# Performance work log

Measured on AMD Instinct MI355X. Metric: run time of the kernel, lower is better.

Reference implementation:

```python
import jax, jax.numpy as jnp
import numpy as np

FEATURE_DIM = 6272
UNITS = 32
B, L = 8, 256

def setup_inputs() -> dict:
    key = jax.random.key(0)
    k1, k2, k3, k4, k5 = jax.random.split(key, 5)
    return {
        "inputs": jax.random.normal(k1, (B, L, FEATURE_DIM), dtype=jnp.float32),
        "Wt": jax.random.normal(k2, (FEATURE_DIM, UNITS), dtype=jnp.float32) * 0.02,
        "bh": jax.random.normal(k3, (UNITS,), dtype=jnp.float32),
        "Wa": jax.random.normal(k4, (UNITS, 1), dtype=jnp.float32) * 0.02,
        "ba": jax.random.normal(k5, (1,), dtype=jnp.float32),
    }

def reference(inputs, Wt, bh, Wa, ba):
    # q == k: both projected through Wt (original code reuses Wt for both)
    p = jnp.einsum('blf,fu->blu', inputs, Wt)            # [B, L, U]
    # additive (Bahdanau-style) pairwise combine: [B, L, L, U]
    beta = jnp.tanh(p[:, :, None, :] + p[:, None, :, :] + bh)
    alpha = jnp.einsum('bqku,uo->bqk', beta, Wa) + ba[0]  # [B, L, L]
    alpha = jax.nn.sigmoid(alpha)
    a = jax.nn.softmax(alpha, axis=-1)                    # softmax over keys
    c_r = jnp.einsum('bqk,bkf->bqf', a, inputs)           # [B, L, F]
    return c_r
```

## Files before the change

kernel.cpp:

```cpp
#include <hip/hip_runtime.h>
#include <hip/hip_bf16.h>
#include <math.h>

#define FDIM 6272
#define LQ   256
#define BN   8
#define UDIM 32
#define BL   (BN*LQ)

typedef short  short8 __attribute__((ext_vector_type(8)));
typedef float  f32x4  __attribute__((ext_vector_type(4)));

static __device__ __forceinline__ ushort f2bf(float f) {
    __hip_bfloat16 h = __float2bfloat16(f);
    return *(ushort*)&h;
}
static __device__ __forceinline__ float fexp2(float x) {
    float r;
    asm volatile("v_exp_f32 %0, %1 \n s_nop 1" : "=v"(r) : "v"(x));
    return r;
}
static __device__ __forceinline__ float frcp(float x) {
    float r;
    asm volatile("v_rcp_f32 %0, %1 \n s_nop 1" : "=v"(r) : "v"(x));
    return r;
}
static __device__ __forceinline__ float tanh_fast(float v) {
    return 1.f - 2.f * frcp(1.f + fexp2(v * 2.88539008177793f));
}

__global__ __launch_bounds__(256)
void k_wtt(const float* __restrict__ Wt, ushort* __restrict__ wtt,
           float* __restrict__ pb) {
    const int gid = blockIdx.x * 256 + threadIdx.x;
    const int u = gid / 784, fg = gid % 784;
    ushort v[8];
    #pragma unroll
    for (int j = 0; j < 8; ++j)
        v[j] = f2bf(Wt[(size_t)(8 * fg + j) * UDIM + u]);
    *(uint4*)(wtt + (size_t)u * FDIM + 8 * fg) = *(uint4*)v;

    if (gid < BL * UDIM / 4)
        ((float4*)pb)[gid] = make_float4(0.f, 0.f, 0.f, 0.f);
}

__global__ __launch_bounds__(256)
void k1_mfma(const float* __restrict__ x, const ushort* __restrict__ wtt,
             float* __restrict__ pb, ushort* __restrict__ xb16) {
    const int t    = threadIdx.x;
    const int wv   = t >> 6, lane = t & 63;
    const int n16  = lane & 15, quad = lane >> 4;
    const int row0 = blockIdx.x * 32 + 16 * (wv & 1);
    const int u0   = 16 * (wv >> 1);
    const int f0   = blockIdx.y * 896;

    const float*  xr = x    + (size_t)(row0 + n16) * FDIM + f0 + quad * 8;
    const ushort* wr = wtt  + (size_t)(u0   + n16) * FDIM + f0 + quad * 8;
    ushort*       xw = xb16 + (size_t)(row0 + n16) * FDIM + f0 + quad * 8;

    f32x4 acc = (f32x4){0.f, 0.f, 0.f, 0.f};

    #pragma unroll 4
    for (int c = 0; c < 28; ++c) {
        const float4 a0 = *(const float4*)(xr + c * 32);
        const float4 a1 = *(const float4*)(xr + c * 32 + 4);
        short8 af;
        af[0] = (short)f2bf(a0.x); af[1] = (short)f2bf(a0.y);
        af[2] = (short)f2bf(a0.z); af[3] = (short)f2bf(a0.w);
        af[4] = (short)f2bf(a1.x); af[5] = (short)f2bf(a1.y);
        af[6] = (short)f2bf(a1.z); af[7] = (short)f2bf(a1.w);
        if (wv < 2)
            *(short8*)(xw + c * 32) = af;
        const short8 bf = *(const short8*)(wr + c * 32);
        acc = __builtin_amdgcn_mfma_f32_16x16x32_bf16(af, bf, acc, 0, 0, 0);
    }

    #pragma unroll
    for (int r = 0; r < 4; ++r)
        atomicAdd(&pb[(size_t)(row0 + quad * 4 + r) * UDIM + u0 + n16], acc[r]);
}

__global__ __launch_bounds__(256)
void k2_attn(const float* __restrict__ pb, const float* __restrict__ bh,
             const float* __restrict__ Wa, const float* __restrict__ ba,
             ushort* __restrict__ ab) {
    const int bq = blockIdx.x;
    const int b  = bq >> 8, q = bq & 255;
    const int k  = threadIdx.x;

    __shared__ float pk_s[LQ * 33];
    __shared__ float pq_s[UDIM];
    __shared__ float wa_s[UDIM];
    __shared__ float red[4];

    if (k < UDIM) wa_s[k] = Wa[k];
    const float* pbb = pb + (size_t)b * LQ * UDIM;
    #pragma unroll
    for (int i = 0; i < 32; ++i) {
        int idx = k + i * 256;
        pk_s[(idx >> 5) * 33 + (idx & 31)] = pbb[idx];
    }
    __syncthreads();
    if (k < UDIM) pq_s[k] = pk_s[q * 33 + k] + bh[k];
    __syncthreads();

    const float* pk = &pk_s[k * 33];
    float s = 0.f;
    #pragma unroll
    for (int u = 0; u < UDIM; ++u)
        s = fmaf(tanh_fast(pq_s[u] + pk[u]), wa_s[u], s);

    const float alpha = frcp(1.f + fexp2(-(s + ba[0]) * 1.44269504088896f));
    const float e = fexp2(alpha * 1.44269504088896f);

    float v = e;
    #pragma unroll
    for (int m = 1; m < 64; m <<= 1) v += __shfl_xor(v, m, 64);
    if ((k & 63) == 0) red[k >> 6] = v;
    __syncthreads();
    const float tot = red[0] + red[1] + red[2] + red[3];

    ab[(size_t)bq * LQ + k] = f2bf(e * frcp(tot));
}

__global__ __launch_bounds__(256)
void k3_fused(const ushort* __restrict__ xb16, const ushort* __restrict__ ab,
              float* __restrict__ out) {
    __shared__ ushort Bs[2][64 * 72];

    const int t    = threadIdx.x;
    const int f0   = blockIdx.x * 64;
    const int b    = blockIdx.y;
    const int wv   = t >> 6;
    const int lane = t & 63;
    const int n16  = lane & 15;
    const int quad = lane >> 4;
    const int g    = t >> 4;
    const int kp   = t & 15;

    const ushort* xb  = xb16 + (size_t)b * LQ * FDIM + f0 + 4 * g;
    const ushort* abb = ab   + (size_t)b * LQ * LQ;

    f32x4 acc[4][4];
    #pragma unroll
    for (int mf = 0; mf < 4; ++mf)
        #pragma unroll
        for (int nf = 0; nf < 4; ++nf)
            acc[mf][nf] = (f32x4){0.f, 0.f, 0.f, 0.f};

    uint2 r0, r1, r2, r3;
#define LDX(kc) do {                                                      \
        r0 = *(const uint2*)(xb + (size_t)((kc) + 2 * kp     ) * FDIM);   \
        r1 = *(const uint2*)(xb + (size_t)((kc) + 2 * kp +  1) * FDIM);   \
        r2 = *(const uint2*)(xb + (size_t)((kc) + 2 * kp + 32) * FDIM);   \
        r3 = *(const uint2*)(xb + (size_t)((kc) + 2 * kp + 33) * FDIM);   \
    } while (0)
#define STX(bufi) do {                                                    \
        unsigned* bw = (unsigned*)(Bs[bufi]);                             \
        bw[(4 * g + 0) * 36 + kp]      = (r0.x & 0xffffu) | (r1.x << 16); \
        bw[(4 * g + 1) * 36 + kp]      = (r0.x >> 16) | (r1.x & 0xffff0000u); \
        bw[(4 * g + 2) * 36 + kp]      = (r0.y & 0xffffu) | (r1.y << 16); \
        bw[(4 * g + 3) * 36 + kp]      = (r0.y >> 16) | (r1.y & 0xffff0000u); \
        bw[(4 * g + 0) * 36 + kp + 16] = (r2.x & 0xffffu) | (r3.x << 16); \
        bw[(4 * g + 1) * 36 + kp + 16] = (r2.x >> 16) | (r3.x & 0xffff0000u); \
        bw[(4 * g + 2) * 36 + kp + 16] = (r2.y & 0xffffu) | (r3.y << 16); \
        bw[(4 * g + 3) * 36 + kp + 16] = (r2.y >> 16) | (r3.y & 0xffff0000u); \
    } while (0)

    LDX(0);
    STX(0);

    for (int c = 0; c < 4; ++c) {
        if (c < 3) LDX((c + 1) * 64);
        short8 af[4][2];
        #pragma unroll
        for (int mf = 0; mf < 4; ++mf)
            #pragma unroll
            for (int h = 0; h < 2; ++h)
                af[mf][h] = *(const short8*)(abb
                    + (size_t)(64 * wv + 16 * mf + n16) * LQ
                    + c * 64 + h * 32 + quad * 8);
        __syncthreads();
        const ushort* bsc = Bs[c & 1];
        #pragma unroll
        for (int h = 0; h < 2; ++h)
            #pragma unroll
            for (int nf = 0; nf < 4; ++nf) {
                const short8 bf = *(const short8*)(bsc + (16 * nf + n16) * 72
                                                   + h * 32 + quad * 8);
                #pragma unroll
                for (int mf = 0; mf < 4; ++mf)
                    acc[mf][nf] = __builtin_amdgcn_mfma_f32_16x16x32_bf16(
                        af[mf][h], bf, acc[mf][nf], 0, 0, 0);
            }
        if (c < 3) STX((c + 1) & 1);
    }
#undef LDX
#undef STX

    float* ob = out + ((size_t)b * LQ + 64 * wv + quad * 4) * FDIM + f0 + n16;
    #pragma unroll
    for (int mf = 0; mf < 4; ++mf)
        #pragma unroll
        for (int nf = 0; nf < 4; ++nf)
            #pragma unroll
            for (int r = 0; r < 4; ++r)
                ob[(size_t)(16 * mf + r) * FDIM + 16 * nf] = acc[mf][nf][r];
}

extern "C" void kernel_launch(void* const* d_in, const int* in_sizes, int n_in,
                              void* d_out, int out_size, void* d_ws, size_t ws_size,
                              hipStream_t stream) {
    const float* x  = (const float*)d_in[0];
    const float* Wt = (const float*)d_in[1];
    const float* bh = (const float*)d_in[2];
    const float* Wa = (const float*)d_in[3];
    const float* ba = (const float*)d_in[4];
    float* out = (float*)d_out;

    float*  pb   = (float*)d_ws;
    ushort* ab   = (ushort*)((char*)d_ws + 262144);
    ushort* wtt  = (ushort*)((char*)d_ws + 262144 + 1048576);
    ushort* xb16 = (ushort*)((char*)d_ws + 262144 + 1048576 + 524288);

    k_wtt<<<98, 256, 0, stream>>>(Wt, wtt, pb);
    k1_mfma<<<dim3(64, 7), 256, 0, stream>>>(x, wtt, pb, xb16);
    k2_attn<<<BL, 256, 0, stream>>>(pb, bh, Wa, ba, ab);
    k3_fused<<<dim3(98, 8), 256, 0, stream>>>(xb16, ab, out);
}
```

Before: 163.1 us.

## Factor tanh via exp products and batch queries per block in attention kernel

The attention-score kernel rewrites tanh(pq+pk+bh) using precomputed exponentials: exp(2pk) is computed once per key and exp(2bh) once per unit, so each pair costs one FMA and one reciprocal instead of an exp plus a reciprocal. Each block now handles four queries per batch, so the key projection staging and exponentials are reused across queries. The projection kernel also splits the feature dimension into twice as many chunks for more parallelism, at the cost of more atomics. The exp-product form can overflow for large projections, which risks inf/NaN handling differences.

```diff
diff --git a/kernel.cpp b/kernel.cpp
--- a/kernel.cpp
+++ b/kernel.cpp
@@ -7,6 +7,7 @@
 #define BN   8
 #define UDIM 32
 #define BL   (BN*LQ)
+#define QG   4
 
 typedef short  short8 __attribute__((ext_vector_type(8)));
 typedef float  f32x4  __attribute__((ext_vector_type(4)));
@@ -24,9 +25,6 @@
     float r;
     asm volatile("v_rcp_f32 %0, %1 \n s_nop 1" : "=v"(r) : "v"(x));
     return r;
-}
-static __device__ __forceinline__ float tanh_fast(float v) {
-    return 1.f - 2.f * frcp(1.f + fexp2(v * 2.88539008177793f));
 }
 
 __global__ __launch_bounds__(256)
@@ -52,7 +50,7 @@
     const int n16  = lane & 15, quad = lane >> 4;
     const int row0 = blockIdx.x * 32 + 16 * (wv & 1);
     const int u0   = 16 * (wv >> 1);
-    const int f0   = blockIdx.y * 896;
+    const int f0   = blockIdx.y * 448;
 
     const float*  xr = x    + (size_t)(row0 + n16) * FDIM + f0 + quad * 8;
     const ushort* wr = wtt  + (size_t)(u0   + n16) * FDIM + f0 + quad * 8;
@@ -60,8 +58,8 @@
 
     f32x4 acc = (f32x4){0.f, 0.f, 0.f, 0.f};
 
-    #pragma unroll 4
-    for (int c = 0; c < 28; ++c) {
+    #pragma unroll 7
+    for (int c = 0; c < 14; ++c) {
         const float4 a0 = *(const float4*)(xr + c * 32);
         const float4 a1 = *(const float4*)(xr + c * 32 + 4);
         short8 af;
@@ -84,43 +82,61 @@
 void k2_attn(const float* __restrict__ pb, const float* __restrict__ bh,
              const float* __restrict__ Wa, const float* __restrict__ ba,
              ushort* __restrict__ ab) {
-    const int bq = blockIdx.x;
-    const int b  = bq >> 8, q = bq & 255;
+    const int b  = blockIdx.y;
+    const int q0 = blockIdx.x * QG;
     const int k  = threadIdx.x;
 
-    __shared__ float pk_s[LQ * 33];
-    __shared__ float pq_s[UDIM];
-    __shared__ float wa_s[UDIM];
+    __shared__ float tk_s[LQ * 33];
+    __shared__ float tq_s[UDIM];
+    __shared__ float wa2_s[UDIM];
+    __shared__ float ebh_s[UDIM];
+    __shared__ float swa_s;
     __shared__ float red[4];
 
-    if (k < UDIM) wa_s[k] = Wa[k];
+    const float KL = 2.88539008177793f;
+
+    if (k < UDIM) { wa2_s[k] = 2.f * Wa[k]; ebh_s[k] = fexp2(KL * bh[k]); }
+    if (k < 64) {
+        float v = (k < UDIM) ? Wa[k] : 0.f;
+        #pragma unroll
+        for (int m = 1; m < 64; m <<= 1) v += __shfl_xor(v, m, 64);
+        if (k == 0) swa_s = v;
+    }
     const float* pbb = pb + (size_t)b * LQ * UDIM;
     #pragma unroll
     for (int i = 0; i < 32; ++i) {
-        int idx = k + i * 256;
-        pk_s[(idx >> 5) * 33 + (idx & 31)] = pbb[idx];
+        const int idx = k + i * 256;
+        tk_s[(idx >> 5) * 33 + (idx & 31)] = fexp2(KL * pbb[idx]);
     }
     __syncthreads();
-    if (k < UDIM) pq_s[k] = pk_s[q * 33 + k] + bh[k];
-    __syncthreads();
-
-    const float* pk = &pk_s[k * 33];
-    float s = 0.f;
-    #pragma unroll
-    for (int u = 0; u < UDIM; ++u)
-        s = fmaf(tanh_fast(pq_s[u] + pk[u]), wa_s[u], s);
-
-    const float alpha = frcp(1.f + fexp2(-(s + ba[0]) * 1.44269504088896f));
-    const float e = fexp2(alpha * 1.44269504088896f);
-
-    float v = e;
-    #pragma unroll
-    for (int m = 1; m < 64; m <<= 1) v += __shfl_xor(v, m, 64);
-    if ((k & 63) == 0) red[k >> 6] = v;
-    __syncthreads();
-    const float tot = red[0] + red[1] + red[2] + red[3];
-
-    ab[(size_t)bq * LQ + k] = f2bf(e * frcp(tot));
+
+    const float  swa = swa_s;
+    const float* tk  = &tk_s[k * 33];
+
+    for (int qi = 0; qi < QG; ++qi) {
+        const int q = q0 + qi;
+        if (k < UDIM) tq_s[k] = ebh_s[k] * tk_s[q * 33 + k];
+        __syncthreads();
+
+        float sacc = 0.f;
+        #pragma unroll
+        for (int u = 0; u < UDIM; ++u)
+            sacc = fmaf(wa2_s[u], frcp(fmaf(tq_s[u], tk[u], 1.f)), sacc);
+        const float s = swa - sacc;
+
+        const float alpha = frcp(1.f + fexp2(-(s + ba[0]) * 1.44269504088896f));
+        const float e = fexp2(alpha * 1.44269504088896f);
+
+        float v = e;
+        #pragma unroll
+        for (int m = 1; m < 64; m <<= 1) v += __shfl_xor(v, m, 64);
+        if ((k & 63) == 0) red[k >> 6] = v;
+        __syncthreads();
+        const float tot = red[0] + red[1] + red[2] + red[3];
+
+        ab[((size_t)b * LQ + q) * LQ + k] = f2bf(e * frcp(tot));
+        __syncthreads();
+    }
 }
 
 __global__ __launch_bounds__(256)
@@ -224,7 +240,7 @@
     ushort* xb16 = (ushort*)((char*)d_ws + 262144 + 1048576 + 524288);
 
     k_wtt<<<98, 256, 0, stream>>>(Wt, wtt, pb);
-    k1_mfma<<<dim3(64, 7), 256, 0, stream>>>(x, wtt, pb, xb16);
-    k2_attn<<<BL, 256, 0, stream>>>(pb, bh, Wa, ba, ab);
+    k1_mfma<<<dim3(64, 14), 256, 0, stream>>>(x, wtt, pb, xb16);
+    k2_attn<<<dim3(LQ / QG, BN), 256, 0, stream>>>(pb, bh, Wa, ba, ab);
     k3_fused<<<dim3(98, 8), 256, 0, stream>>>(xb16, ab, out);
 }
```

Result: slower. 170.5 us (+4.5%).
